# Performance work log

Measured on AMD Instinct MI355X. Metric: run time of the kernel, lower is better.

Reference implementation:

```python
import jax, jax.numpy as jnp
import numpy as np

NUM_HEADS = 16
ROPE_BASE = 10000.0


def _rope_interleaved(x, cos, sin):
    # x: [B,S,H,Hd]; cos/sin: [S,Hd/2]. Interleaved pairs (even, odd).
    x1 = x[..., 0::2]
    x2 = x[..., 1::2]
    c = cos[None, :, None, :]
    s = sin[None, :, None, :]
    o1 = x1 * c - x2 * s
    o2 = x1 * s + x2 * c
    return jnp.stack([o1, o2], axis=-1).reshape(x.shape)


def setup_inputs() -> dict:
    key = jax.random.key(0)
    ks = jax.random.split(key, 5)
    B, S, D = 2, 2048, 2048
    init_scale = 0.02
    x = jax.random.normal(ks[0], (B, S, D), jnp.float32)
    Wq = jax.random.normal(ks[1], (D, D), jnp.float32) * init_scale
    Wk = jax.random.normal(ks[2], (D, D), jnp.float32) * init_scale
    Wv = jax.random.normal(ks[3], (D, D), jnp.float32) * init_scale
    Wo = jax.random.normal(ks[4], (D, D), jnp.float32) * init_scale
    return {"x": x, "Wq": Wq, "Wk": Wk, "Wv": Wv, "Wo": Wo}


def reference(x, Wq, Wk, Wv, Wo):
    B, S, D = x.shape
    H = NUM_HEADS
    Hd = D // H
    # QKV projections (bias-free)
    q = (x @ Wq).reshape(B, S, H, Hd)
    k = (x @ Wk).reshape(B, S, H, Hd)
    v = (x @ Wv).reshape(B, S, H, Hd)
    # Rotary embedding, interleaved, base 10000, full head_dim
    pos = jnp.arange(S, dtype=jnp.float32)
    inv_freq = 1.0 / (ROPE_BASE ** (jnp.arange(0, Hd, 2, dtype=jnp.float32) / Hd))
    angles = pos[:, None] * inv_freq[None, :]  # [S, Hd/2]
    cos, sin = jnp.cos(angles), jnp.sin(angles)
    q = _rope_interleaved(q, cos, sin)
    k = _rope_interleaved(k, cos, sin)
    # Causal scaled-dot-product attention (flash_attn_func default scale = Hd**-0.5)
    scale = Hd ** -0.5
    scores = jnp.einsum('bqhd,bkhd->bhqk', q, k) * scale
    causal = jnp.tril(jnp.ones((S, S), dtype=bool))
    scores = jnp.where(causal[None, None], scores, jnp.finfo(scores.dtype).min)
    probs = jax.nn.softmax(scores, axis=-1)
    attn = jnp.einsum('bhqk,bkhd->bqhd', probs, v).reshape(B, S, D)
    return attn @ Wo
```

## Files before the change

### kernel.cpp

```cpp
#include <hip/hip_runtime.h>
#include <hip/hip_bf16.h>

static constexpr int BB = 2;
static constexpr int SS = 2048;
static constexpr int DD = 2048;
static constexpr int HH = 16;
static constexpr int HD = 128;

typedef __bf16 bf16_t;
typedef __bf16 bf16x8 __attribute__((ext_vector_type(8)));
typedef __bf16 bf16x4 __attribute__((ext_vector_type(4)));
typedef float  floatx4 __attribute__((ext_vector_type(4)));

__device__ __forceinline__ void gl2lds16(const bf16_t* g, bf16_t* l) {
    __builtin_amdgcn_global_load_lds(
        (const __attribute__((address_space(1))) void*)g,
        (__attribute__((address_space(3))) void*)l, 16, 0, 0);
}

__global__ void cast_x_kernel(const float* __restrict__ x, bf16_t* __restrict__ xb) {
    int i = blockIdx.x * 256 + threadIdx.x;
    float4 v = ((const float4*)x)[i];
    bf16x4 o;
    o.x = (bf16_t)v.x; o.y = (bf16_t)v.y; o.z = (bf16_t)v.z; o.w = (bf16_t)v.w;
    ((bf16x4*)xb)[i] = o;
}

__global__ void transpose_cast_kernel(const float* __restrict__ W, bf16_t* __restrict__ Wt) {
    __shared__ float tile[32][33];
    int bx = blockIdx.x * 32;
    int by = blockIdx.y * 32;
    int tx = threadIdx.x, ty = threadIdx.y;
#pragma unroll
    for (int j = 0; j < 4; ++j)
        tile[ty + j * 8][tx] = W[(size_t)(by + ty + j * 8) * DD + bx + tx];
    __syncthreads();
#pragma unroll
    for (int j = 0; j < 4; ++j)
        Wt[(size_t)(bx + ty + j * 8) * DD + by + tx] = (bf16_t)tile[tx][ty + j * 8];
}

template <int MODE>
__global__ __launch_bounds__(256, 2) void gemm_bt_kernel(
    const bf16_t* __restrict__ A, const bf16_t* __restrict__ Bt,
    float* __restrict__ Cf, bf16_t* __restrict__ Qw, bf16_t* __restrict__ Kw,
    bf16_t* __restrict__ Vw, int N, int K) {
    __shared__ __align__(16) bf16_t As[128 * 64];
    __shared__ __align__(16) bf16_t Bs[128 * 64];

    const int t = threadIdx.x;
    const int lane = t & 63;
    const int wave = t >> 6;
    const int lrow = lane & 15;
    const int lkq  = lane >> 4;
    const int wm = (wave & 1) * 64;
    const int wn = (wave >> 1) * 64;
    const int m0 = blockIdx.y * 128;
    const int n0 = blockIdx.x * 128;

    floatx4 acc[4][4];
#pragma unroll
    for (int i = 0; i < 4; ++i)
#pragma unroll
        for (int j = 0; j < 4; ++j) acc[i][j] = (floatx4)0.0f;

    const int srow  = lane >> 3;
    const int sch   = (lane & 7) ^ srow;

    for (int k0 = 0; k0 < K; k0 += 64) {
        __syncthreads();
#pragma unroll
        for (int p = 0; p < 4; ++p) {
            int r = wave * 32 + p * 8 + srow;
            gl2lds16(A  + (size_t)(m0 + r) * K + k0 + sch * 8, As + (wave * 32 + p * 8) * 64);
            gl2lds16(Bt + (size_t)(n0 + r) * K + k0 + sch * 8, Bs + (wave * 32 + p * 8) * 64);
        }
        __syncthreads();
#pragma unroll
        for (int ks = 0; ks < 2; ++ks) {
            bf16x8 af[4], bg[4];
#pragma unroll
            for (int i = 0; i < 4; ++i) {
                int pos = ((ks * 4 + lkq) ^ (lrow & 7)) * 8;
                af[i] = *(const bf16x8*)(As + (wm + i * 16 + lrow) * 64 + pos);
                bg[i] = *(const bf16x8*)(Bs + (wn + i * 16 + lrow) * 64 + pos);
            }
#pragma unroll
            for (int i = 0; i < 4; ++i)
#pragma unroll
                for (int j = 0; j < 4; ++j)
                    acc[i][j] = __builtin_amdgcn_mfma_f32_16x16x32_bf16(af[i], bg[j], acc[i][j], 0, 0, 0);
        }
    }

#pragma unroll
    for (int i = 0; i < 4; ++i)
#pragma unroll
        for (int j = 0; j < 4; ++j)
#pragma unroll
            for (int r = 0; r < 4; ++r) {
                int m = m0 + wm + i * 16 + lkq * 4 + r;
                int n = n0 + wn + j * 16 + lrow;
                float v = acc[i][j][r];
                if (MODE == 1) {
                    Cf[(size_t)m * N + n] = v;
                } else {
                    bf16_t bv = (bf16_t)v;
                    int b = m >> 11, s = m & (SS - 1);
                    int nn = n & (DD - 1);
                    int h = nn >> 7, d = nn & 127;
                    size_t off = (((size_t)b * HH + h) * SS + s) * HD + d;
                    if (n < DD)            Qw[off] = bv;
                    else if (n < 2 * DD)   Kw[off] = bv;
                    else                   Vw[off] = bv;
                }
            }
}

__global__ void rope_kernel(bf16_t* __restrict__ Qw, bf16_t* __restrict__ Kw) {
    int idx = blockIdx.x * 256 + threadIdx.x;
    int i  = idx & 63;
    int s  = (idx >> 6) & (SS - 1);
    int bh = idx >> 17;
    float inv = expf(-(float)(2 * i) * (9.210340371976184f / 128.0f));
    float ang = (float)s * inv;
    float c = cosf(ang), sn = sinf(ang);
    size_t base = ((size_t)bh * SS + s) * HD + 2 * i;
    float q1 = (float)Qw[base], q2 = (float)Qw[base + 1];
    Qw[base]     = (bf16_t)(q1 * c - q2 * sn);
    Qw[base + 1] = (bf16_t)(q1 * sn + q2 * c);
    float k1 = (float)Kw[base], k2 = (float)Kw[base + 1];
    Kw[base]     = (bf16_t)(k1 * c - k2 * sn);
    Kw[base + 1] = (bf16_t)(k1 * sn + k2 * c);
}

__global__ void vtrans_kernel(const bf16_t* __restrict__ Vw, bf16_t* __restrict__ Vt) {
    __shared__ unsigned short lds[64][65];
    const int t = threadIdx.x;
    const int s0 = blockIdx.x * 64, d0 = blockIdx.y * 64, bh = blockIdx.z;
    const bf16_t* src = Vw + ((size_t)bh * SS + s0) * HD + d0;
    bf16_t* dst = Vt + ((size_t)bh * HD + d0) * SS + s0;
#pragma unroll
    for (int p = 0; p < 2; ++p) {
        int c = p * 256 + t;
        int s = c >> 3, ch = c & 7;
        uint4 v = *(const uint4*)(src + (size_t)s * HD + ch * 8);
        const unsigned short* pv = (const unsigned short*)&v;
#pragma unroll
        for (int e = 0; e < 8; ++e) lds[ch * 8 + e][s] = pv[e];
    }
    __syncthreads();
    {
        int d = t >> 2, sb = (t & 3) * 16;
        uint4 o[2];
        unsigned short* po = (unsigned short*)o;
#pragma unroll
        for (int e = 0; e < 16; ++e) po[e] = lds[d][sb + e];
        *(uint4*)(dst + (size_t)d * SS + sb) = o[0];
        *(uint4*)(dst + (size_t)d * SS + sb + 8) = o[1];
    }
}

__global__ __launch_bounds__(256, 2) void flash_attn_kernel(
    const bf16_t* __restrict__ Qw, const bf16_t* __restrict__ Kw,
    const bf16_t* __restrict__ Vtw, bf16_t* __restrict__ Attn) {
    __shared__ __align__(16) bf16_t Ks[64 * 128];
    __shared__ __align__(16) bf16_t Vs[128 * 64];
    __shared__ __align__(16) bf16_t Ps[4][16 * 72];

    const int t = threadIdx.x;
    const int lane = t & 63;
    const int wave = t >> 6;
    const int lrow = lane & 15;
    const int lkq  = lane >> 4;
    const int bx = blockIdx.x;
    const int qtile = (bx & 1) ? (bx >> 1) : (15 - (bx >> 1));
    const int bh = blockIdx.y;
    const int q0 = qtile * 128;

    const bf16_t* Qbh = Qw + (size_t)bh * SS * HD;
    const bf16_t* Kbh = Kw + (size_t)bh * SS * HD;
    const bf16_t* Vbh = Vtw + (size_t)bh * HD * SS;

    const int qb[2] = { q0 + wave * 16, q0 + 64 + wave * 16 };

    const float qscale = 0.08838834764831845f * 1.4426950408889634f;
    bf16x8 qf[2][4];
#pragma unroll
    for (int qs = 0; qs < 2; ++qs)
#pragma unroll
        for (int kc4 = 0; kc4 < 4; ++kc4) {
            qf[qs][kc4] = *(const bf16x8*)(Qbh + (size_t)(qb[qs] + lrow) * HD + kc4 * 32 + lkq * 8);
#pragma unroll
            for (int e = 0; e < 8; ++e) qf[qs][kc4][e] = (bf16_t)((float)qf[qs][kc4][e] * qscale);
        }

    floatx4 oacc[2][8];
#pragma unroll
    for (int qs = 0; qs < 2; ++qs)
#pragma unroll
        for (int i = 0; i < 8; ++i) oacc[qs][i] = (floatx4)0.0f;
    float m_i[2] = { -1e30f, -1e30f };
    float l_i[2] = { 0.0f, 0.0f };

    const int nch = 2 * qtile + 2;
    for (int kc = 0; kc < nch; ++kc) {
        __syncthreads();
#pragma unroll
        for (int p = 0; p < 4; ++p) {
            int row = wave * 16 + p * 4 + (lane >> 4);
            int gch = (lane & 15) ^ (row & 7);
            gl2lds16(Kbh + (size_t)(kc * 64 + row) * HD + gch * 8,
                     Ks + (wave * 16 + p * 4) * 128);
        }
#pragma unroll
        for (int p = 0; p < 4; ++p) {
            int row = wave * 32 + p * 8 + (lane >> 3);
            int gch = (lane & 7) ^ (row & 7);
            gl2lds16(Vbh + (size_t)row * SS + kc * 64 + gch * 8,
                     Vs + (wave * 32 + p * 8) * 64);
        }
        __syncthreads();

        const bool act0 = (kc * 64 <= qb[0] + 15);

        floatx4 sacc[2][4];
#pragma unroll
        for (int qs = 0; qs < 2; ++qs)
#pragma unroll
            for (int i = 0; i < 4; ++i) sacc[qs][i] = (floatx4)0.0f;
#pragma unroll
        for (int nf = 0; nf < 4; ++nf)
#pragma unroll
            for (int kc4 = 0; kc4 < 4; ++kc4) {
                bf16x8 kf = *(const bf16x8*)(Ks + (nf * 16 + lrow) * 128 +
                                             (((kc4 * 4 + lkq) ^ (lrow & 7)) * 8));
                if (act0)
                    sacc[0][nf] = __builtin_amdgcn_mfma_f32_16x16x32_bf16(kf, qf[0][kc4], sacc[0][nf], 0, 0, 0);
                sacc[1][nf] = __builtin_amdgcn_mfma_f32_16x16x32_bf16(kf, qf[1][kc4], sacc[1][nf], 0, 0, 0);
            }

        bf16x8 pa[2][2];
#pragma unroll
        for (int qs = 0; qs < 2; ++qs) {
            const int qbase = qb[qs];
            if (qs == 0 && !act0) continue;

            const int qg = qbase + lrow;
            float mx = m_i[qs];
            if (kc * 64 + 63 > qbase) {
#pragma unroll
                for (int nf = 0; nf < 4; ++nf)
#pragma unroll
                    for (int r = 0; r < 4; ++r) {
                        int kg = kc * 64 + nf * 16 + lkq * 4 + r;
                        float sv = (kg > qg) ? -1e30f : sacc[qs][nf][r];
                        sacc[qs][nf][r] = sv;
                        mx = fmaxf(mx, sv);
                    }
            } else {
#pragma unroll
                for (int nf = 0; nf < 4; ++nf)
#pragma unroll
                    for (int r = 0; r < 4; ++r) mx = fmaxf(mx, sacc[qs][nf][r]);
            }
            mx = fmaxf(mx, __shfl_xor(mx, 16));
            mx = fmaxf(mx, __shfl_xor(mx, 32));
            float alpha = exp2f(m_i[qs] - mx);
            m_i[qs] = mx;

            float rs = 0.0f;
#pragma unroll
            for (int nf = 0; nf < 4; ++nf)
#pragma unroll
                for (int r = 0; r < 4; ++r) {
                    float pv = exp2f(sacc[qs][nf][r] - mx);
                    sacc[qs][nf][r] = pv;
                    rs += pv;
                }
            rs += __shfl_xor(rs, 16);
            rs += __shfl_xor(rs, 32);
            l_i[qs] = l_i[qs] * alpha + rs;

            if (__ballot(alpha < 1.0f)) {
                float av[4];
#pragma unroll
                for (int r = 0; r < 4; ++r) av[r] = __shfl(alpha, lkq * 4 + r);
#pragma unroll
                for (int nf8 = 0; nf8 < 8; ++nf8)
#pragma unroll
                    for (int r = 0; r < 4; ++r) oacc[qs][nf8][r] *= av[r];
            }

#pragma unroll
            for (int nf = 0; nf < 4; ++nf) {
                bf16x4 pk;
#pragma unroll
                for (int r = 0; r < 4; ++r) pk[r] = (bf16_t)sacc[qs][nf][r];
                *(bf16x4*)(Ps[wave] + lrow * 72 + nf * 16 + lkq * 4) = pk;
            }
#pragma unroll
            for (int k2 = 0; k2 < 2; ++k2)
                pa[qs][k2] = *(const bf16x8*)(Ps[wave] + lrow * 72 + k2 * 32 + lkq * 8);
        }

#pragma unroll
        for (int nf8 = 0; nf8 < 8; ++nf8)
#pragma unroll
            for (int k2 = 0; k2 < 2; ++k2) {
                bf16x8 vf = *(const bf16x8*)(Vs + (nf8 * 16 + lrow) * 64 +
                                             (((k2 * 4 + lkq) ^ (lrow & 7)) * 8));
                if (act0)
                    oacc[0][nf8] = __builtin_amdgcn_mfma_f32_16x16x32_bf16(pa[0][k2], vf, oacc[0][nf8], 0, 0, 0);
                oacc[1][nf8] = __builtin_amdgcn_mfma_f32_16x16x32_bf16(pa[1][k2], vf, oacc[1][nf8], 0, 0, 0);
            }
    }

    int bb = bh >> 4, h = bh & 15;
#pragma unroll
    for (int qs = 0; qs < 2; ++qs)
#pragma unroll
        for (int r = 0; r < 4; ++r) {
            float invl = 1.0f / __shfl(l_i[qs], lkq * 4 + r);
            int q = qb[qs] + lkq * 4 + r;
#pragma unroll
            for (int nf8 = 0; nf8 < 8; ++nf8)
                Attn[((size_t)bb * SS + q) * DD + h * HD + nf8 * 16 + lrow] =
                    (bf16_t)(oacc[qs][nf8][r] * invl);
        }
}

extern "C" void kernel_launch(void* const* d_in, const int* in_sizes, int n_in,
                              void* d_out, int out_size, void* d_ws, size_t ws_size,
                              hipStream_t stream) {
    const float* x  = (const float*)d_in[0];
    const float* Wq = (const float*)d_in[1];
    const float* Wk = (const float*)d_in[2];
    const float* Wv = (const float*)d_in[3];
    const float* Wo = (const float*)d_in[4];
    float* out = (float*)d_out;

    bf16_t* p = (bf16_t*)d_ws;
    bf16_t* Xb    = p; p += (size_t)BB * SS * DD;
    bf16_t* Wqkvt = p; p += (size_t)3 * DD * DD;
    bf16_t* Wot   = p; p += (size_t)DD * DD;
    bf16_t* Qw    = p; p += (size_t)BB * HH * SS * HD;
    bf16_t* Kw    = p; p += (size_t)BB * HH * SS * HD;
    bf16_t* Vtw   = p; p += (size_t)BB * HH * SS * HD;
    bf16_t* Attn  = p; p += (size_t)BB * SS * DD;
    bf16_t* Vw = Attn;

    cast_x_kernel<<<(BB * SS * DD / 4) / 256, 256, 0, stream>>>(x, Xb);

    dim3 tb(32, 8), tg(DD / 32, DD / 32);
    transpose_cast_kernel<<<tg, tb, 0, stream>>>(Wq, Wqkvt);
    transpose_cast_kernel<<<tg, tb, 0, stream>>>(Wk, Wqkvt + (size_t)DD * DD);
    transpose_cast_kernel<<<tg, tb, 0, stream>>>(Wv, Wqkvt + (size_t)2 * DD * DD);
    transpose_cast_kernel<<<tg, tb, 0, stream>>>(Wo, Wot);

    gemm_bt_kernel<0><<<dim3(3 * DD / 128, BB * SS / 128), 256, 0, stream>>>(
        Xb, Wqkvt, nullptr, Qw, Kw, Vw, 3 * DD, DD);

    rope_kernel<<<(BB * HH * SS * 64) / 256, 256, 0, stream>>>(Qw, Kw);

    vtrans_kernel<<<dim3(SS / 64, HD / 64, BB * HH), 256, 0, stream>>>(Vw, Vtw);

    flash_attn_kernel<<<dim3(SS / 128, BB * HH), 256, 0, stream>>>(Qw, Kw, Vtw, Attn);

    gemm_bt_kernel<1><<<dim3(DD / 128, BB * SS / 128), 256, 0, stream>>>(
        Attn, Wot, out, nullptr, nullptr, nullptr, DD, DD);
}
```

Baseline: 416.3 us.

## Double-buffer K/V tiles in LDS to prefetch the next chunk during compute

```diff
diff --git a/kernel.cpp b/kernel.cpp
--- a/kernel.cpp
+++ b/kernel.cpp
@@ -164,8 +164,8 @@
 __global__ __launch_bounds__(256, 2) void flash_attn_kernel(
     const bf16_t* __restrict__ Qw, const bf16_t* __restrict__ Kw,
     const bf16_t* __restrict__ Vtw, bf16_t* __restrict__ Attn) {
-    __shared__ __align__(16) bf16_t Ks[64 * 128];
-    __shared__ __align__(16) bf16_t Vs[128 * 64];
+    __shared__ __align__(16) bf16_t Ks[2][64 * 128];
+    __shared__ __align__(16) bf16_t Vs[2][128 * 64];
     __shared__ __align__(16) bf16_t Ps[4][16 * 72];
 
     const int t = threadIdx.x;
@@ -184,6 +184,9 @@
 
     const int qb[2] = { q0 + wave * 16, q0 + 64 + wave * 16 };
 
+    const int krow = wave * 16 + (lane >> 4);
+    const int vrow = wave * 32 + (lane >> 3);
+
     const float qscale = 0.08838834764831845f * 1.4426950408889634f;
     bf16x8 qf[2][4];
 #pragma unroll
@@ -204,24 +207,43 @@
     float l_i[2] = { 0.0f, 0.0f };
 
     const int nch = 2 * qtile + 2;
+
+#pragma unroll
+    for (int p = 0; p < 4; ++p) {
+        int row = krow + p * 4;
+        int gch = (lane & 15) ^ (row & 7);
+        gl2lds16(Kbh + (size_t)row * HD + gch * 8, Ks[0] + (wave * 16 + p * 4) * 128);
+    }
+#pragma unroll
+    for (int p = 0; p < 4; ++p) {
+        int row = vrow + p * 8;
+        int gch = (lane & 7) ^ (row & 7);
+        gl2lds16(Vbh + (size_t)row * SS + gch * 8, Vs[0] + (wave * 32 + p * 8) * 64);
+    }
+
+    int cur = 0;
     for (int kc = 0; kc < nch; ++kc) {
         __syncthreads();
-#pragma unroll
-        for (int p = 0; p < 4; ++p) {
-            int row = wave * 16 + p * 4 + (lane >> 4);
-            int gch = (lane & 15) ^ (row & 7);
-            gl2lds16(Kbh + (size_t)(kc * 64 + row) * HD + gch * 8,
-                     Ks + (wave * 16 + p * 4) * 128);
-        }
-#pragma unroll
-        for (int p = 0; p < 4; ++p) {
-            int row = wave * 32 + p * 8 + (lane >> 3);
-            int gch = (lane & 7) ^ (row & 7);
-            gl2lds16(Vbh + (size_t)row * SS + kc * 64 + gch * 8,
-                     Vs + (wave * 32 + p * 8) * 64);
-        }
-        __syncthreads();
-
+
+        if (kc + 1 < nch) {
+            const int nb = cur ^ 1;
+            const size_t kco = (size_t)(kc + 1) * 64;
+#pragma unroll
+            for (int p = 0; p < 4; ++p) {
+                int row = krow + p * 4;
+                int gch = (lane & 15) ^ (row & 7);
+                gl2lds16(Kbh + (kco + row) * HD + gch * 8, Ks[nb] + (wave * 16 + p * 4) * 128);
+            }
+#pragma unroll
+            for (int p = 0; p < 4; ++p) {
+                int row = vrow + p * 8;
+                int gch = (lane & 7) ^ (row & 7);
+                gl2lds16(Vbh + (size_t)row * SS + kco + gch * 8, Vs[nb] + (wave * 32 + p * 8) * 64);
+            }
+        }
+
+        const bf16_t* Ksc = Ks[cur];
+        const bf16_t* Vsc = Vs[cur];
         const bool act0 = (kc * 64 <= qb[0] + 15);
 
         floatx4 sacc[2][4];
@@ -233,7 +255,7 @@
         for (int nf = 0; nf < 4; ++nf)
 #pragma unroll
             for (int kc4 = 0; kc4 < 4; ++kc4) {
-                bf16x8 kf = *(const bf16x8*)(Ks + (nf * 16 + lrow) * 128 +
+                bf16x8 kf = *(const bf16x8*)(Ksc + (nf * 16 + lrow) * 128 +
                                              (((kc4 * 4 + lkq) ^ (lrow & 7)) * 8));
                 if (act0)
                     sacc[0][nf] = __builtin_amdgcn_mfma_f32_16x16x32_bf16(kf, qf[0][kc4], sacc[0][nf], 0, 0, 0);
@@ -308,12 +330,14 @@
         for (int nf8 = 0; nf8 < 8; ++nf8)
 #pragma unroll
             for (int k2 = 0; k2 < 2; ++k2) {
-                bf16x8 vf = *(const bf16x8*)(Vs + (nf8 * 16 + lrow) * 64 +
+                bf16x8 vf = *(const bf16x8*)(Vsc + (nf8 * 16 + lrow) * 64 +
                                              (((k2 * 4 + lkq) ^ (lrow & 7)) * 8));
                 if (act0)
                     oacc[0][nf8] = __builtin_amdgcn_mfma_f32_16x16x32_bf16(pa[0][k2], vf, oacc[0][nf8], 0, 0, 0);
                 oacc[1][nf8] = __builtin_amdgcn_mfma_f32_16x16x32_bf16(pa[1][k2], vf, oacc[1][nf8], 0, 0, 0);
             }
+
+        cur ^= 1;
     }
 
     int bb = bh >> 4, h = bh & 15;
```

After: 420.6 us. Within noise of the previous version (+1.1%).
